# Performance work log

Measured on AMD Instinct MI355X. Metric: run time of the kernel, lower is better.

## Reference

```python
import jax, jax.numpy as jnp
import numpy as np

B, T, D, H, DK = 4, 2048, 1024, 16, 64
DV = 2 * DK
QKD = H * DK           # 1024
VD = H * DV            # 2048
KW = 4                 # conv kernel size
EPS = 1e-5


def zc_rms(x, scale):
    # zero-centered RMS norm over last axis
    xc = x - jnp.mean(x, axis=-1, keepdims=True)
    return xc * jax.lax.rsqrt(jnp.mean(xc * xc, axis=-1, keepdims=True) + EPS) * scale


def causal_dwconv(x, kern, bias):
    # depthwise causal conv1d: x [B,T,C], kern [K,C], bias [C]
    k = kern.shape[0]
    t = x.shape[1]
    xp = jnp.pad(x, ((0, 0), (k - 1, 0), (0, 0)))
    out = bias
    for i in range(k):  # small fixed K=4
        out = out + xp[:, i:i + t, :] * kern[i]
    return out


def _forward(x, q_w, k_w, v_w, q_scale, k_scale, v_scale,
             q_conv_k, q_conv_b, k_conv_k, k_conv_b, v_conv_k, v_conv_b,
             alpha_w, beta_w, out_w, gate_w):
    # Q/K/V: Dense -> zero-centered RMSNorm -> causal depthwise conv -> SiLU
    q = jax.nn.silu(causal_dwconv(zc_rms(x @ q_w, q_scale), q_conv_k, q_conv_b))
    k = jax.nn.silu(causal_dwconv(zc_rms(x @ k_w, k_scale), k_conv_k, k_conv_b))
    v = jax.nn.silu(causal_dwconv(zc_rms(x @ v_w, v_scale), v_conv_k, v_conv_b))

    q = q.reshape(B, T, H, DK)
    k = k.reshape(B, T, H, DK)
    v = v.reshape(B, T, H, DV)

    alpha = jax.nn.sigmoid(x @ alpha_w)  # [B,T,H] per-head decay gate
    beta = jax.nn.sigmoid(x @ beta_w)    # [B,T,H] per-head write strength

    def step(S, inp):
        # S: [B,H,DK,DV]
        qt, kt, vt, at, bt = inp
        Sd = at[..., None, None] * S                              # gated decay
        pred = jnp.einsum('bhd,bhdv->bhv', kt, Sd)                # current memory readout at k
        S_new = Sd + bt[..., None, None] * jnp.einsum('bhd,bhv->bhdv', kt, vt - pred)  # delta rule
        ot = jnp.einsum('bhd,bhdv->bhv', qt, S_new)
        return S_new, ot

    xs = (jnp.transpose(q, (1, 0, 2, 3)),
          jnp.transpose(k, (1, 0, 2, 3)),
          jnp.transpose(v, (1, 0, 2, 3)),
          jnp.transpose(alpha, (1, 0, 2)),
          jnp.transpose(beta, (1, 0, 2)))
    S0 = jnp.zeros((B, H, DK, DV), x.dtype)
    _, o = jax.lax.scan(step, S0, xs)                             # o: [T,B,H,DV]

    core = jnp.transpose(o, (1, 0, 2, 3)).reshape(B, T, VD)
    # gated linear unit output
    return (core @ out_w) * jax.nn.sigmoid(x @ gate_w)


def setup_inputs() -> dict:
    key = jax.random.key(0)
    ks = jax.random.split(key, 12)
    g = lambda i, shape, s: jax.random.normal(ks[i], shape, dtype=jnp.float32) * s
    return {
        'x': g(0, (B, T, D), 1.0),
        'q_w': g(1, (D, QKD), 0.02), 'k_w': g(2, (D, QKD), 0.02), 'v_w': g(3, (D, VD), 0.02),
        'q_scale': jnp.ones((QKD,), jnp.float32),
        'k_scale': jnp.ones((QKD,), jnp.float32),
        'v_scale': jnp.ones((VD,), jnp.float32),
        'q_conv_k': g(4, (KW, QKD), 0.1), 'q_conv_b': jnp.zeros((QKD,), jnp.float32),
        'k_conv_k': g(5, (KW, QKD), 0.1), 'k_conv_b': jnp.zeros((QKD,), jnp.float32),
        'v_conv_k': g(6, (KW, VD), 0.1), 'v_conv_b': jnp.zeros((VD,), jnp.float32),
        'alpha_w': g(7, (D, H), 0.02), 'beta_w': g(8, (D, H), 0.02),
        'out_w': g(9, (VD, D), 0.02), 'gate_w': g(10, (D, D), 0.02),
    }


def reference(x, q_w, k_w, v_w, q_scale, k_scale, v_scale,
              q_conv_k, q_conv_b, k_conv_k, k_conv_b, v_conv_k, v_conv_b,
              alpha_w, beta_w, out_w, gate_w):
    return _forward(x, q_w, k_w, v_w, q_scale, k_scale, v_scale,
                    q_conv_k, q_conv_b, k_conv_k, k_conv_b, v_conv_k, v_conv_b,
                    alpha_w, beta_w, out_w, gate_w)
```

## Files before the change

kernel.cpp:

```cpp
#include <hip/hip_runtime.h>

#define Bc   4
#define Tc   2048
#define Dc   1024
#define Hc   16
#define DKc  64
#define DVc  128
#define QKDc 1024
#define VDc  2048
#define NPRJ 5120
#define Mc   (Bc * Tc)
#define CHUNK 64
#define NCHK (Tc / CHUNK)

typedef __bf16 bf16;
typedef __bf16 bf16x4 __attribute__((ext_vector_type(4)));
typedef __bf16 bf16x8 __attribute__((ext_vector_type(8)));
typedef float  f32x4  __attribute__((ext_vector_type(4)));

__device__ __forceinline__ float bf2f(bf16 v) { return (float)v; }
__device__ __forceinline__ bf16  f2bf(float v) { return (bf16)v; }
__device__ __forceinline__ float sigmoidf_(float x) { return 1.0f / (1.0f + __expf(-x)); }
__device__ __forceinline__ f32x4 mfma16(bf16x8 a, bf16x8 b, f32x4 c) {
    return __builtin_amdgcn_mfma_f32_16x16x32_bf16(a, b, c, 0, 0, 0);
}

__device__ __forceinline__ void glds16(const bf16* g, void* l) {
    __builtin_amdgcn_global_load_lds((const __attribute__((address_space(1))) void*)g,
                                     (__attribute__((address_space(3))) void*)l, 16, 0, 0);
}

__device__ __forceinline__ bf16* swz32x64(bf16* base, int r, int k) {
    int byte = (((r << 6) + k) << 1) ^ ((r & 7) << 4);
    return (bf16*)((char*)base + byte);
}

__global__ __launch_bounds__(256) void cast_f32_bf16(const float* __restrict__ src,
                                                     bf16* __restrict__ dst, int n4) {
    int i = blockIdx.x * 256 + threadIdx.x;
    if (i < n4) {
        float4 v = ((const float4*)src)[i];
        bf16x4 o = { f2bf(v.x), f2bf(v.y), f2bf(v.z), f2bf(v.w) };
        ((bf16x4*)dst)[i] = o;
    }
}

__global__ __launch_bounds__(256) void transpose_cast(const float* __restrict__ src,
                                                      bf16* __restrict__ dst,
                                                      int R, int C) {
    __shared__ float tile[32][33];
    int c0 = blockIdx.x * 32, r0 = blockIdx.y * 32;
    int tx = threadIdx.x, ty = threadIdx.y;
#pragma unroll
    for (int i = 0; i < 32; i += 8) {
        int r = r0 + ty + i, c = c0 + tx;
        tile[ty + i][tx] = (r < R && c < C) ? src[(size_t)r * C + c] : 0.0f;
    }
    __syncthreads();
#pragma unroll
    for (int i = 0; i < 32; i += 8) {
        int rr = c0 + ty + i, cc = r0 + tx;
        if (rr < C && cc < R) dst[(size_t)rr * R + cc] = f2bf(tile[tx][ty + i]);
    }
}

#define GP_NT 20
#define GP_MT 32
#define GP_NKT 32
__global__ __launch_bounds__(512, 2) void gemm_pipe(const bf16* __restrict__ A,
                                                    const bf16* __restrict__ Bt,
                                                    bf16* __restrict__ C) {
    __shared__ __align__(16) char lds[131072];
    const int tid = threadIdx.x;
    const int wid = tid >> 6, lane = tid & 63;
    const int lm = lane & 15, lq = lane >> 4;
    const int wm = wid >> 2, wn = wid & 3;

    const int id = blockIdx.x;
    const int nid = (id & 7) * ((GP_NT * GP_MT) / 8) + (id >> 3);
    const int tn = nid % GP_NT, tm = nid / GP_NT;
    const int n0 = tn * 256, m0 = tm * 256;

    const int r0 = tid >> 2;
    const int lsx = ((tid & 3) ^ (r0 & 3)) << 3;
    const bf16* sA0 = A  + (size_t)(m0 + r0) * Dc + lsx;
    const bf16* sA1 = sA0 + (size_t)128 * Dc;
    const bf16* sB0 = Bt + (size_t)(n0 + r0) * Dc + lsx;
    const bf16* sB1 = sB0 + (size_t)128 * Dc;

    auto stageA = [&](int kt) {
        char* d = lds + ((kt & 3) << 15) + wid * 1024;
        glds16(sA0 + kt * 32, d);
        glds16(sA1 + kt * 32, d + 8192);
    };
    auto stageB = [&](int kt) {
        char* d = lds + ((kt & 3) << 15) + 16384 + wid * 1024;
        glds16(sB0 + kt * 32, d);
        glds16(sB1 + kt * 32, d + 8192);
    };

    f32x4 acc[8][4] = {};
    const int sx = (lq ^ (lm & 3)) << 3;
    const int aoff = wm * 4096 + lm * 32 + sx;
    const int boff = wn * 2048 + lm * 32 + sx;

    stageA(0); stageB(0); stageA(1); stageB(1); stageA(2); stageB(2);
    asm volatile("s_waitcnt vmcnt(8)" ::: "memory");
    asm volatile("s_barrier" ::: "memory");

    for (int kt = 0; kt < GP_NKT; kt++) {
        const bf16* sA = (const bf16*)(lds + ((kt & 3) << 15));
        const bf16* sB = (const bf16*)(lds + ((kt & 3) << 15) + 16384);
        bf16x8 aF[4], bF[4], aG[4];
#pragma unroll
        for (int i = 0; i < 4; i++) aF[i] = *(const bf16x8*)&sA[aoff + i * 512];
#pragma unroll
        for (int j = 0; j < 4; j++) bF[j] = *(const bf16x8*)&sB[boff + j * 512];
#pragma unroll
        for (int i = 0; i < 4; i++) aG[i] = *(const bf16x8*)&sA[aoff + (i + 4) * 512];
        if (kt + 3 < GP_NKT) { stageA(kt + 3); stageB(kt + 3); }
        __builtin_amdgcn_s_setprio(1);
#pragma unroll
        for (int i = 0; i < 4; i++)
#pragma unroll
            for (int j = 0; j < 4; j++)
                acc[i][j] = mfma16(aF[i], bF[j], acc[i][j]);
#pragma unroll
        for (int i = 0; i < 4; i++)
#pragma unroll
            for (int j = 0; j < 4; j++)
                acc[i + 4][j] = mfma16(aG[i], bF[j], acc[i + 4][j]);
        __builtin_amdgcn_s_setprio(0);
        if (kt + 3 < GP_NKT)      asm volatile("s_waitcnt vmcnt(8)" ::: "memory");
        else if (kt + 2 < GP_NKT) asm volatile("s_waitcnt vmcnt(4)" ::: "memory");
        else                      asm volatile("s_waitcnt vmcnt(0)" ::: "memory");
        asm volatile("s_barrier" ::: "memory");
    }

    const int rbase = m0 + wm * 128 + lq * 4;
    const int cbase = n0 + wn * 64 + lm;
#pragma unroll
    for (int i = 0; i < 8; i++)
#pragma unroll
        for (int j = 0; j < 4; j++)
#pragma unroll
            for (int rI = 0; rI < 4; rI++)
                C[(size_t)(rbase + i * 16 + rI) * NPRJ + cbase + j * 16] =
                    f2bf(acc[i][j][rI]);
}

#define GO_NKT 64
__global__ __launch_bounds__(512, 2) void gemm_pipe_out(const bf16* __restrict__ A,
                                                        const bf16* __restrict__ Bt,
                                                        float* __restrict__ C,
                                                        const bf16* __restrict__ gate) {
    __shared__ __align__(16) char lds[98304];
    const int tid = threadIdx.x;
    const int wid = tid >> 6, lane = tid & 63;
    const int lm = lane & 15, lq = lane >> 4;
    const int wm = wid >> 2, wn = wid & 3;

    const int id = blockIdx.x;
    const int nid = (id & 7) * 32 + (id >> 3);
    const int tm = nid >> 2, tn = nid & 3;
    const int m0 = tm * 128, n0 = tn * 256;

    const int r0 = tid >> 2;
    const int lsx = ((tid & 3) ^ (r0 & 3)) << 3;
    const bf16* sAp = A  + (size_t)(m0 + r0) * NPRJ + lsx;
    const bf16* sB0 = Bt + (size_t)(n0 + r0) * VDc + lsx;
    const bf16* sB1 = sB0 + (size_t)128 * VDc;

    auto stageA = [&](int kt) {
        glds16(sAp + kt * 32, lds + (kt & 3) * 24576 + wid * 1024);
    };
    auto stageB = [&](int kt) {
        char* d = lds + (kt & 3) * 24576 + 8192 + wid * 1024;
        glds16(sB0 + kt * 32, d);
        glds16(sB1 + kt * 32, d + 8192);
    };

    f32x4 acc[4][4] = {};
    const int sx = (lq ^ (lm & 3)) << 3;
    const int aoff = wm * 2048 + lm * 32 + sx;
    const int boff = wn * 2048 + lm * 32 + sx;

    stageA(0); stageB(0); stageA(1); stageB(1); stageA(2); stageB(2);
    asm volatile("s_waitcnt vmcnt(6)" ::: "memory");
    asm volatile("s_barrier" ::: "memory");

    for (int kt = 0; kt < GO_NKT; kt++) {
        const bf16* sA = (const bf16*)(lds + (kt & 3) * 24576);
        const bf16* sB = sA + 4096;
        bf16x8 a[4], b[4];
#pragma unroll
        for (int i = 0; i < 4; i++) a[i] = *(const bf16x8*)&sA[aoff + i * 512];
#pragma unroll
        for (int j = 0; j < 4; j++) b[j] = *(const bf16x8*)&sB[boff + j * 512];
        if (kt + 3 < GO_NKT) { stageA(kt + 3); stageB(kt + 3); }
        __builtin_amdgcn_s_setprio(1);
#pragma unroll
        for (int i = 0; i < 4; i++)
#pragma unroll
            for (int j = 0; j < 4; j++)
                acc[i][j] = mfma16(a[i], b[j], acc[i][j]);
        __builtin_amdgcn_s_setprio(0);
        if (kt + 3 < GO_NKT)      asm volatile("s_waitcnt vmcnt(6)" ::: "memory");
        else if (kt + 2 < GO_NKT) asm volatile("s_waitcnt vmcnt(3)" ::: "memory");
        else                      asm volatile("s_waitcnt vmcnt(0)" ::: "memory");
        asm volatile("s_barrier" ::: "memory");
    }

    const int rbase = m0 + wm * 64 + lq * 4;
    const int cbase = n0 + wn * 64 + lm;
#pragma unroll
    for (int i = 0; i < 4; i++)
#pragma unroll
        for (int j = 0; j < 4; j++)
#pragma unroll
            for (int rI = 0; rI < 4; rI++) {
                int row = rbase + i * 16 + rI;
                int col = cbase + j * 16;
                float g = bf2f(gate[(size_t)row * NPRJ + col]);
                C[(size_t)row * Dc + col] = acc[i][j][rI] * sigmoidf_(g);
            }
}

template <int L>
__global__ __launch_bounds__(256) void zc_rms_v(bf16* __restrict__ buf,
                                                const float* __restrict__ scale,
                                                int ld) {
    constexpr int NW = L / 8 / 64;
    const int row = blockIdx.x, t = threadIdx.x;
    bf16* p = buf + (size_t)row * ld;
    bf16x8 v = *(const bf16x8*)&p[t * 8];
    float xv[8], s = 0.f, s2 = 0.f;
#pragma unroll
    for (int e = 0; e < 8; e++) { xv[e] = bf2f(v[e]); s += xv[e]; s2 += xv[e] * xv[e]; }
    __shared__ float red[2][NW];
#pragma unroll
    for (int o = 32; o > 0; o >>= 1) {
        s += __shfl_down(s, o, 64);
        s2 += __shfl_down(s2, o, 64);
    }
    if ((t & 63) == 0) { red[0][t >> 6] = s; red[1][t >> 6] = s2; }
    __syncthreads();
    s = 0.f; s2 = 0.f;
#pragma unroll
    for (int wv = 0; wv < NW; wv++) { s += red[0][wv]; s2 += red[1][wv]; }
    float mean = s / (float)L;
    float inv = rsqrtf(s2 / (float)L - mean * mean + 1e-5f);
    float4 s0 = *(const float4*)&scale[t * 8];
    float4 s1 = *(const float4*)&scale[t * 8 + 4];
    float sc[8] = { s0.x, s0.y, s0.z, s0.w, s1.x, s1.y, s1.z, s1.w };
    bf16x8 o;
#pragma unroll
    for (int e = 0; e < 8; e++) o[e] = f2bf((xv[e] - mean) * inv * sc[e]);
    *(bf16x8*)&p[t * 8] = o;
}

template <int CCH>
__global__ __launch_bounds__(256) void conv_silu_v(const bf16* __restrict__ xn,
                                                   const float* __restrict__ kern,
                                                   const float* __restrict__ bias,
                                                   bf16* __restrict__ out, int ldin) {
    const int btok = blockIdx.x;
    const int tt = btok & (Tc - 1);
    const int c8 = threadIdx.x * 8;
    float4 b0 = *(const float4*)&bias[c8], b1 = *(const float4*)&bias[c8 + 4];
    float acc[8] = { b0.x, b0.y, b0.z, b0.w, b1.x, b1.y, b1.z, b1.w };
#pragma unroll
    for (int i = 0; i < 4; i++) {
        if (tt - 3 + i >= 0) {
            bf16x8 xv = *(const bf16x8*)&xn[(size_t)(btok - 3 + i) * ldin + c8];
            float4 k0 = *(const float4*)&kern[i * CCH + c8];
            float4 k1 = *(const float4*)&kern[i * CCH + c8 + 4];
            float kk[8] = { k0.x, k0.y, k0.z, k0.w, k1.x, k1.y, k1.z, k1.w };
#pragma unroll
            for (int e = 0; e < 8; e++) acc[e] += bf2f(xv[e]) * kk[e];
        }
    }
    bf16x8 o;
#pragma unroll
    for (int e = 0; e < 8; e++) {
        float y = acc[e] * sigmoidf_(acc[e]);
        o[e] = f2bf(y);
    }
    *(bf16x8*)&out[(size_t)btok * CCH + c8] = o;
}

__global__ __launch_bounds__(256) void alphabeta_mfma(const bf16* __restrict__ x,
                                                      const float* __restrict__ aw,
                                                      const float* __restrict__ bw,
                                                      float* __restrict__ af,
                                                      float* __restrict__ bfv) {
    __shared__ bf16 whi[32][136];
    __shared__ bf16 wlo[32][136];
    const int tid = threadIdx.x, wave = tid >> 6, lane = tid & 63;
    const int lm = lane & 15, lq = lane >> 4;
    const int m0 = blockIdx.x * 128;
    f32x4 acc[2][2] = {};

    for (int k0 = 0; k0 < Dc; k0 += 128) {
        for (int idx = tid; idx < 4096; idx += 256) {
            int n = idx & 31, kk = idx >> 5;
            float v = (n < 16) ? aw[(size_t)(k0 + kk) * Hc + n]
                               : bw[(size_t)(k0 + kk) * Hc + (n - 16)];
            bf16 h = f2bf(v);
            whi[n][kk] = h;
            wlo[n][kk] = f2bf(v - bf2f(h));
        }
        __syncthreads();
#pragma unroll
        for (int ks = 0; ks < 4; ks++) {
            bf16x8 bh[2], bl[2];
#pragma unroll
            for (int j = 0; j < 2; j++) {
                bh[j] = *(const bf16x8*)&whi[j * 16 + lm][ks * 32 + lq * 8];
                bl[j] = *(const bf16x8*)&wlo[j * 16 + lm][ks * 32 + lq * 8];
            }
#pragma unroll
            for (int ii = 0; ii < 2; ii++) {
                int row = m0 + wave * 32 + ii * 16 + lm;
                bf16x8 a = *(const bf16x8*)&x[(size_t)row * Dc + k0 + ks * 32 + lq * 8];
#pragma unroll
                for (int j = 0; j < 2; j++) {
                    acc[ii][j] = mfma16(a, bh[j], acc[ii][j]);
                    acc[ii][j] = mfma16(a, bl[j], acc[ii][j]);
                }
            }
        }
        __syncthreads();
    }
#pragma unroll
    for (int ii = 0; ii < 2; ii++)
#pragma unroll
        for (int rI = 0; rI < 4; rI++) {
            int row = m0 + wave * 32 + ii * 16 + lq * 4 + rI;
            af[(size_t)row * Hc + lm]  = sigmoidf_(acc[ii][0][rI]);
            bfv[(size_t)row * Hc + lm] = sigmoidf_(acc[ii][1][rI]);
        }
}

__global__ __launch_bounds__(256) void prep(bf16* __restrict__ qf,
                                            bf16* __restrict__ kf,
                                            bf16* __restrict__ vc,
                                            const float* __restrict__ af,
                                            const float* __restrict__ bfv,
                                            bf16* __restrict__ Wb,
                                            bf16* __restrict__ Mb,
                                            float* __restrict__ gamC) {
    __shared__ __align__(16) char smem[53248];
    bf16*  Kc   = (bf16*)(smem);
    bf16*  Qc   = (bf16*)(smem + 9216);
    float* DT   = (float*)(smem + 9216);
    float* Pn   = (float*)(smem + 13568);
    float* TT   = (float*)(smem + 15744);
    float* Qn   = (float*)(smem + 9216);
    bf16*  Tb   = (bf16*)(smem + 9216);
    float* As   = (float*)(smem + 18432);
    bf16*  Vtb  = (bf16*)(smem + 18432);
    float* Ts   = (float*)(smem + 35072);
    float* lg_s = (float*)(smem + 51712);
    float* bv_s = lg_s + 64;
    float* bg_s = lg_s + 128;
    float* gm_s = lg_s + 192;
    float* kr_s = lg_s + 256;

    const int c    = blockIdx.x;
    const int bh   = blockIdx.y;
    const int b    = bh >> 4, h = bh & 15;
    const int ch   = bh * NCHK + c;
    const int tok0 = b * Tc + c * CHUNK;
    const int tid  = threadIdx.x;
    const int wave = tid >> 6, lane = tid & 63;
    const int lm = lane & 15, lq = lane >> 4, kh = lq * 8;

#pragma unroll
    for (int r = 0; r < 2; r++) {
        int idx = tid + r * 256;
        int row = idx >> 3, c8 = (idx & 7) * 8;
        *(bf16x8*)&Kc[row * 72 + c8] =
            *(const bf16x8*)&kf[(size_t)(tok0 + row) * QKDc + h * DKc + c8];
        *(bf16x8*)&Qc[row * 72 + c8] =
            *(const bf16x8*)&qf[(size_t)(tok0 + row) * QKDc + h * DKc + c8];
    }
    for (int idx = tid; idx < 64 * 65; idx += 256) Ts[idx] = 0.f;
    if (tid < 64) {
        float a  = af[(size_t)(tok0 + tid) * Hc + h];
        float bb = bfv[(size_t)(tok0 + tid) * Hc + h];
        float la = __log2f(fmaxf(a, 1e-30f));
#pragma unroll
        for (int o = 1; o < 64; o <<= 1) {
            float t = __shfl_up(la, o, 64);
            if (tid >= o) la += t;
        }
        float lgC = __shfl(la, 63, 64);
        lg_s[tid] = la;
        bv_s[tid] = bb;
        float g   = exp2f(la);
        gm_s[tid] = g;
        bg_s[tid] = bb * g;
        kr_s[tid] = exp2f(lgC - la);
        if (tid == 0) gamC[ch] = exp2f(lgC);
    }
    __syncthreads();

    {
        bf16x8 ka[2], qa[2];
#pragma unroll
        for (int s = 0; s < 2; s++) {
            ka[s] = *(const bf16x8*)&Kc[(16 * wave + lm) * 72 + s * 32 + kh];
            qa[s] = *(const bf16x8*)&Qc[(16 * wave + lm) * 72 + s * 32 + kh];
        }
#pragma unroll
        for (int jt = 0; jt < 4; jt++) {
            f32x4 kkacc = {}, qkacc = {};
#pragma unroll
            for (int s = 0; s < 2; s++) {
                bf16x8 kbf = *(const bf16x8*)&Kc[(16 * jt + lm) * 72 + s * 32 + kh];
                kkacc = mfma16(ka[s], kbf, kkacc);
                qkacc = mfma16(qa[s], kbf, qkacc);
            }
#pragma unroll
            for (int rI = 0; rI < 4; rI++) {
                int i = 16 * wave + lq * 4 + rI;
                int j = 16 * jt + lm;
                float ratio = exp2f(lg_s[i] - lg_s[j]);
                As[i * 65 + j] = (j < i) ? bv_s[i] * ratio * kkacc[rI] : 0.f;
                Mb[((size_t)ch * 64 + i) * 64 + j] =
                    (j <= i) ? f2bf(ratio * qkacc[rI]) : f2bf(0.f);
            }
        }
    }
    {
#pragma unroll
        for (int r = 0; r < 2; r++) {
            int idx = tid + r * 256;
            int row = idx >> 3, c8 = (idx & 7) * 8;
            bf16x8 v = *(const bf16x8*)&Qc[row * 72 + c8];
            float g = gm_s[row];
            bf16x8 oq;
#pragma unroll
            for (int e = 0; e < 8; e++) oq[e] = f2bf(bf2f(v[e]) * g);
            *(bf16x8*)&qf[(size_t)(tok0 + row) * QKDc + h * DKc + c8] = oq;
            bf16x8 ok;
#pragma unroll
            for (int e = 0; e < 8; e++)
                ok[e] = f2bf(kr_s[c8 + e] * bf2f(Kc[(c8 + e) * 72 + row]));
            *(bf16x8*)&kf[(size_t)(tok0 + row) * QKDc + h * DKc + c8] = ok;
        }
    }
    __syncthreads();

    if (tid < 64) {
        const int g = lane >> 4, jj = lane & 15, base = lane & 48;
        float areg[16], tcol[16];
#pragma unroll
        for (int i = 0; i < 16; i++) areg[i] = As[(16 * g + i) * 65 + 16 * g + jj];
#pragma unroll
        for (int i = 0; i < 16; i++) tcol[i] = (i == jj) ? 1.f : 0.f;
#pragma unroll
        for (int i = 1; i < 16; i++) {
            float s = 0.f;
#pragma unroll
            for (int m = 0; m < i; m++)
                s = fmaf(__shfl(areg[i], base + m, 64), tcol[m], s);
            tcol[i] = (i == jj) ? 1.f : -s;
        }
#pragma unroll
        for (int i = 0; i < 16; i++) {
            Ts[(16 * g + i) * 65 + 16 * g + jj] = tcol[i];
            DT[g * 272 + jj * 17 + i] = tcol[i];
        }
    }
    __syncthreads();

    if (wave < 2) {
        const int w = wave;
        bf16x8 ah, al, bh, bl;
#pragma unroll
        for (int e = 0; e < 8; e++) {
            int k = kh + e;
            float xa = (k < 16) ? DT[2 * w * 272 + lm * 17 + k] : 0.f;
            bf16 ha = f2bf(xa); ah[e] = ha; al[e] = f2bf(xa - bf2f(ha));
            float xb = (k < 16) ? As[(16 + 32 * w + lm) * 65 + 32 * w + k] : 0.f;
            bf16 hb = f2bf(xb); bh[e] = hb; bl[e] = f2bf(xb - bf2f(hb));
        }
        f32x4 acc = {};
        acc = mfma16(ah, bh, acc); acc = mfma16(ah, bl, acc); acc = mfma16(al, bh, acc);
#pragma unroll
        for (int rI = 0; rI < 4; rI++)
            Pn[w * 272 + (lq * 4 + rI) * 17 + lm] = -acc[rI];
    }
    __syncthreads();

    if (wave < 3) {
        bf16x8 ah, al, bh, bl;
#pragma unroll
        for (int e = 0; e < 8; e++) {
            int k = kh + e;
            float xa = 0.f, xb = 0.f;
            if (k < 16) {
                if (wave == 0)      { xa = Ts[(16 + lm) * 65 + 16 + k]; xb = Pn[lm * 17 + k]; }
                else if (wave == 1) { xa = Pn[lm * 17 + k];             xb = Ts[(16 + lm) * 65 + 16 + k]; }
                else                { xa = Ts[(48 + lm) * 65 + 48 + k]; xb = Pn[272 + lm * 17 + k]; }
            }
            bf16 ha = f2bf(xa); ah[e] = ha; al[e] = f2bf(xa - bf2f(ha));
            bf16 hb = f2bf(xb); bh[e] = hb; bl[e] = f2bf(xb - bf2f(hb));
        }
        f32x4 acc = {};
        acc = mfma16(ah, bh, acc); acc = mfma16(ah, bl, acc); acc = mfma16(al, bh, acc);
#pragma unroll
        for (int rI = 0; rI < 4; rI++) {
            int ro = lq * 4 + rI;
            if (wave == 0)      Ts[(16 + ro) * 65 + lm]      = acc[rI];
            else if (wave == 1) TT[ro * 17 + lm]             = acc[rI];
            else                Ts[(48 + ro) * 65 + 32 + lm] = acc[rI];
        }
    }
    __syncthreads();

    {
        const int a = wave >> 1, bq = wave & 1;
        bf16x8 ah, al, bh, bl;
#pragma unroll
        for (int e = 0; e < 8; e++) {
            int k = kh + e;
            float xa;
            if (a == 0) xa = (k < 16) ? DT[lm * 17 + k] : TT[lm * 17 + (k - 16)];
            else        xa = (k < 16) ? 0.f : DT[272 + lm * 17 + (k - 16)];
            bf16 ha = f2bf(xa); ah[e] = ha; al[e] = f2bf(xa - bf2f(ha));
            float xb = As[(32 + 16 * bq + lm) * 65 + k];
            bf16 hb = f2bf(xb); bh[e] = hb; bl[e] = f2bf(xb - bf2f(hb));
        }
        f32x4 acc = {};
        acc = mfma16(ah, bh, acc); acc = mfma16(ah, bl, acc); acc = mfma16(al, bh, acc);
        __syncthreads();
#pragma unroll
        for (int rI = 0; rI < 4; rI++)
            Qn[(16 * a + lq * 4 + rI) * 33 + 16 * bq + lm] = -acc[rI];
    }
    __syncthreads();

    {
        const int a = wave >> 1, bq = wave & 1;
        bf16x8 ah, al, bh, bl;
#pragma unroll
        for (int e = 0; e < 8; e++) {
            int k = kh + e;
            float xa = Ts[(32 + 16 * a + lm) * 65 + 32 + k];
            bf16 ha = f2bf(xa); ah[e] = ha; al[e] = f2bf(xa - bf2f(ha));
            float xb = Qn[(16 * bq + lm) * 33 + k];
            bf16 hb = f2bf(xb); bh[e] = hb; bl[e] = f2bf(xb - bf2f(hb));
        }
        f32x4 acc = {};
        acc = mfma16(ah, bh, acc); acc = mfma16(ah, bl, acc); acc = mfma16(al, bh, acc);
#pragma unroll
        for (int rI = 0; rI < 4; rI++)
            Ts[(32 + 16 * a + lq * 4 + rI) * 65 + 16 * bq + lm] = acc[rI];
    }
    __syncthreads();

    for (int idx = tid; idx < 4096; idx += 256) {
        int i = idx >> 6, j = idx & 63;
        Tb[i * 72 + j] = f2bf(Ts[i * 65 + j]);
    }
    __syncthreads();
#pragma unroll
    for (int r = 0; r < 4; r++) {
        int idx = tid + r * 256;
        int j = idx >> 4, c8 = (idx & 15) * 8;
        bf16x8 v = *(const bf16x8*)&vc[(size_t)(tok0 + j) * VDc + h * DVc + c8];
        float bb = bv_s[j];
#pragma unroll
        for (int e = 0; e < 8; e++)
            Vtb[(c8 + e) * 72 + j] = f2bf(bf2f(v[e]) * bb);
    }
    __syncthreads();
    {
        bf16x8 ta[2];
#pragma unroll
        for (int s = 0; s < 2; s++)
            ta[s] = *(const bf16x8*)&Tb[(16 * wave + lm) * 72 + s * 32 + kh];
#pragma unroll
        for (int dt = 0; dt < 4; dt++) {
            f32x4 wacc = {};
#pragma unroll
            for (int s = 0; s < 2; s++) {
                bf16x8 wbf;
                int d = 16 * dt + lm;
#pragma unroll
                for (int e = 0; e < 8; e++) {
                    int j = s * 32 + kh + e;
                    wbf[e] = f2bf(bg_s[j] * bf2f(Kc[j * 72 + d]));
                }
                wacc = mfma16(ta[s], wbf, wacc);
            }
#pragma unroll
            for (int rI = 0; rI < 4; rI++) {
                int i = 16 * wave + lq * 4 + rI;
                Wb[((size_t)ch * 64 + i) * 64 + 16 * dt + lm] = f2bf(wacc[rI]);
            }
        }
#pragma unroll
        for (int dt = 0; dt < 8; dt++) {
            f32x4 uacc = {};
#pragma unroll
            for (int s = 0; s < 2; s++) {
                bf16x8 vb = *(const bf16x8*)&Vtb[(16 * dt + lm) * 72 + s * 32 + kh];
                uacc = mfma16(ta[s], vb, uacc);
            }
#pragma unroll
            for (int rI = 0; rI < 4; rI++) {
                int i = 16 * wave + lq * 4 + rI;
                vc[(size_t)(tok0 + i) * VDc + h * DVc + 16 * dt + lm] = f2bf(uacc[rI]);
            }
        }
    }
}

__global__ __launch_bounds__(256) void chunkloop(const bf16* __restrict__ qf,
                                                 const bf16* __restrict__ kf,
                                                 const bf16* __restrict__ vc,
                                                 const bf16* __restrict__ Wb,
                                                 const bf16* __restrict__ Mb,
                                                 const float* __restrict__ gamC,
                                                 bf16* __restrict__ o, int ldo) {
    const int vg = blockIdx.x;
    const int bh = blockIdx.y;
    const int b = bh >> 4, h = bh & 15;
    const int tid = threadIdx.x;
    const int wave = tid >> 6, lane = tid & 63;
    const int lm = lane & 15, lq = lane >> 4, kh = lq * 8;

    __shared__ __align__(16) bf16 SbBuf[32 * 64];
    __shared__ __align__(16) bf16 UtBuf[32 * 64];

    for (int idx = tid; idx < 32 * 64; idx += 256) SbBuf[idx] = f2bf(0.f);

    f32x4 Sacc[2] = {};

    const int colK = h * DKc;
    const int colV = h * DVc + vg * 32;

    bf16x8 wa[2], qa[2], ma[2], kb[2];
    bf16 uvv[2][4];

    auto loadFrags = [&](int c, bf16x8 (&wa_)[2], bf16x8 (&qa_)[2], bf16x8 (&ma_)[2],
                         bf16x8 (&kb_)[2], bf16 (&uvv_)[2][4]) {
        const int tok0 = b * Tc + c * CHUNK;
        const size_t chb = ((size_t)bh * NCHK + c) * 64;
#pragma unroll
        for (int s = 0; s < 2; s++) {
            wa_[s] = *(const bf16x8*)&Wb[(chb + 16 * wave + lm) * 64 + s * 32 + kh];
            ma_[s] = *(const bf16x8*)&Mb[(chb + 16 * wave + lm) * 64 + s * 32 + kh];
            qa_[s] = *(const bf16x8*)&qf[(size_t)(tok0 + 16 * wave + lm) * QKDc + colK + s * 32 + kh];
            kb_[s] = *(const bf16x8*)&kf[(size_t)(tok0 + 16 * wave + lm) * QKDc + colK + s * 32 + kh];
        }
#pragma unroll
        for (int dt = 0; dt < 2; dt++)
#pragma unroll
            for (int rI = 0; rI < 4; rI++)
                uvv_[dt][rI] =
                    vc[(size_t)(tok0 + 16 * wave + lq * 4 + rI) * VDc + colV + 16 * dt + lm];
    };

    loadFrags(0, wa, qa, ma, kb, uvv);
    __syncthreads();

    for (int c = 0; c < NCHK; c++) {
        const float gC = gamC[(size_t)bh * NCHK + c];
        bf16x8 sf[2][2];
#pragma unroll
        for (int dt = 0; dt < 2; dt++)
#pragma unroll
            for (int s = 0; s < 2; s++)
                sf[dt][s] = *(const bf16x8*)swz32x64(SbBuf, 16 * dt + lm, s * 32 + kh);
        f32x4 pacc[2] = {};
#pragma unroll
        for (int dt = 0; dt < 2; dt++)
#pragma unroll
            for (int s = 0; s < 2; s++)
                pacc[dt] = mfma16(wa[s], sf[dt][s], pacc[dt]);

        bf16x8 wa2[2], qa2[2], ma2[2], kb2[2];
        bf16 uvv2[2][4];
        if (c + 1 < NCHK) loadFrags(c + 1, wa2, qa2, ma2, kb2, uvv2);

#pragma unroll
        for (int dt = 0; dt < 2; dt++)
#pragma unroll
            for (int rI = 0; rI < 4; rI++) {
                float u = bf2f(uvv[dt][rI]) - pacc[dt][rI];
                *swz32x64(UtBuf, 16 * dt + lm, 16 * wave + lq * 4 + rI) = f2bf(u);
            }
        __syncthreads();

        bf16x8 uf[2][2];
#pragma unroll
        for (int dt = 0; dt < 2; dt++)
#pragma unroll
            for (int s = 0; s < 2; s++)
                uf[dt][s] = *(const bf16x8*)swz32x64(UtBuf, 16 * dt + lm, s * 32 + kh);

        f32x4 oacc[2] = {};
#pragma unroll
        for (int dt = 0; dt < 2; dt++)
#pragma unroll
            for (int s = 0; s < 2; s++) {
                oacc[dt] = mfma16(qa[s], sf[dt][s], oacc[dt]);
                oacc[dt] = mfma16(ma[s], uf[dt][s], oacc[dt]);
            }
        {
            const int tok0 = b * Tc + c * CHUNK;
#pragma unroll
            for (int dt = 0; dt < 2; dt++)
#pragma unroll
                for (int rI = 0; rI < 4; rI++)
                    o[(size_t)(tok0 + 16 * wave + lq * 4 + rI) * ldo + colV + 16 * dt + lm] =
                        f2bf(oacc[dt][rI]);
        }
#pragma unroll
        for (int dt = 0; dt < 2; dt++) {
#pragma unroll
            for (int e = 0; e < 4; e++) Sacc[dt][e] *= gC;
#pragma unroll
            for (int s = 0; s < 2; s++)
                Sacc[dt] = mfma16(uf[dt][s], kb[s], Sacc[dt]);
        }
        __syncthreads();
#pragma unroll
        for (int dt = 0; dt < 2; dt++)
#pragma unroll
            for (int rI = 0; rI < 4; rI++)
                *swz32x64(SbBuf, 16 * dt + lq * 4 + rI, 16 * wave + lm) = f2bf(Sacc[dt][rI]);
        __syncthreads();

        if (c + 1 < NCHK) {
#pragma unroll
            for (int s = 0; s < 2; s++) { wa[s] = wa2[s]; qa[s] = qa2[s]; ma[s] = ma2[s]; kb[s] = kb2[s]; }
#pragma unroll
            for (int dt = 0; dt < 2; dt++)
#pragma unroll
                for (int rI = 0; rI < 4; rI++) uvv[dt][rI] = uvv2[dt][rI];
        }
    }
}

extern "C" void kernel_launch(void* const* d_in, const int* in_sizes, int n_in,
                              void* d_out, int out_size, void* d_ws, size_t ws_size,
                              hipStream_t stream) {
    const float* x        = (const float*)d_in[0];
    const float* q_w      = (const float*)d_in[1];
    const float* k_w      = (const float*)d_in[2];
    const float* v_w      = (const float*)d_in[3];
    const float* q_scale  = (const float*)d_in[4];
    const float* k_scale  = (const float*)d_in[5];
    const float* v_scale  = (const float*)d_in[6];
    const float* q_conv_k = (const float*)d_in[7];
    const float* q_conv_b = (const float*)d_in[8];
    const float* k_conv_k = (const float*)d_in[9];
    const float* k_conv_b = (const float*)d_in[10];
    const float* v_conv_k = (const float*)d_in[11];
    const float* v_conv_b = (const float*)d_in[12];
    const float* alpha_w  = (const float*)d_in[13];
    const float* beta_w   = (const float*)d_in[14];
    const float* out_w    = (const float*)d_in[15];
    const float* gate_w   = (const float*)d_in[16];

    char* w = (char*)d_ws;
    bf16* xb  = (bf16*)w; w += (size_t)Mc * Dc * 2;
    bf16* qwT = (bf16*)w; w += (size_t)QKDc * Dc * 2;
    bf16* kwT = (bf16*)w; w += (size_t)QKDc * Dc * 2;
    bf16* vwT = (bf16*)w; w += (size_t)VDc * Dc * 2;
    bf16* gwT = (bf16*)w; w += (size_t)Dc * Dc * 2;
    bf16* owT = (bf16*)w; w += (size_t)Dc * VDc * 2;
    bf16* lin_all = (bf16*)w; w += (size_t)Mc * NPRJ * 2;
    bf16* qf = (bf16*)w; w += (size_t)Mc * QKDc * 2;
    bf16* kf = (bf16*)w; w += (size_t)Mc * QKDc * 2;
    bf16* vc = (bf16*)w; w += (size_t)Mc * VDc * 2;
    float* af = (float*)w; w += (size_t)Mc * Hc * 4;
    float* bfv = (float*)w; w += (size_t)Mc * Hc * 4;
    const int NCH_TOT = Bc * Hc * NCHK;
    bf16* Wb = (bf16*)w; w += (size_t)NCH_TOT * 64 * 64 * 2;
    bf16* Mb = (bf16*)w; w += (size_t)NCH_TOT * 64 * 64 * 2;
    float* gamC = (float*)w; w += (size_t)NCH_TOT * 4;
    bf16* o_core = lin_all;

    dim3 tb(32, 8);
    cast_f32_bf16<<<(Mc * Dc / 4 + 255) / 256, 256, 0, stream>>>(x, xb, Mc * Dc / 4);
    transpose_cast<<<dim3(QKDc / 32, Dc / 32), tb, 0, stream>>>(q_w, qwT, Dc, QKDc);
    transpose_cast<<<dim3(QKDc / 32, Dc / 32), tb, 0, stream>>>(k_w, kwT, Dc, QKDc);
    transpose_cast<<<dim3(VDc / 32, Dc / 32), tb, 0, stream>>>(v_w, vwT, Dc, VDc);
    transpose_cast<<<dim3(Dc / 32, Dc / 32), tb, 0, stream>>>(gate_w, gwT, Dc, Dc);
    transpose_cast<<<dim3(Dc / 32, VDc / 32), tb, 0, stream>>>(out_w, owT, VDc, Dc);

    gemm_pipe<<<GP_NT * GP_MT, 512, 0, stream>>>(xb, qwT, lin_all);

    zc_rms_v<QKDc><<<Mc, QKDc / 8, 0, stream>>>(lin_all,        q_scale, NPRJ);
    zc_rms_v<QKDc><<<Mc, QKDc / 8, 0, stream>>>(lin_all + 1024, k_scale, NPRJ);
    zc_rms_v<VDc><<<Mc, VDc / 8, 0, stream>>>(lin_all + 2048,   v_scale, NPRJ);

    conv_silu_v<QKDc><<<Mc, QKDc / 8, 0, stream>>>(lin_all,        q_conv_k, q_conv_b, qf, NPRJ);
    conv_silu_v<QKDc><<<Mc, QKDc / 8, 0, stream>>>(lin_all + 1024, k_conv_k, k_conv_b, kf, NPRJ);
    conv_silu_v<VDc><<<Mc, VDc / 8, 0, stream>>>(lin_all + 2048,   v_conv_k, v_conv_b, vc, NPRJ);

    alphabeta_mfma<<<Mc / 128, 256, 0, stream>>>(xb, alpha_w, beta_w, af, bfv);

    prep<<<dim3(NCHK, Bc * Hc), 256, 0, stream>>>(qf, kf, vc, af, bfv, Wb, Mb, gamC);
    chunkloop<<<dim3(4, Bc * Hc), 256, 0, stream>>>(qf, kf, vc, Wb, Mb, gamC, o_core, NPRJ);

    gemm_pipe_out<<<256, 512, 0, stream>>>(o_core, owT, (float*)d_out, lin_all + 4096);
}
```

Measured before the change: 524.5 us.

## Fuse RMS norm into conv, retune LDS swizzle, remap chunkloop blocks and V transpose

Merges the zero-centered RMS norm and the causal conv+SiLU into one kernel. Each block recomputes the norm statistics for the 4 rows in the conv window, so the in-place normalized write and the separate launches go away. It also changes the XOR swizzle in both GEMMs to use row bits 1-2, which should cut LDS bank conflicts. The chunkloop grid becomes 1D with an XCD-aware mapping so blocks sharing a head land on the same XCD, and the prep V-transpose load pattern is reordered. The fused kernel does four times the reductions per row, so it adds redundant compute and register pressure.

```diff
diff --git a/kernel.cpp b/kernel.cpp
--- a/kernel.cpp
+++ b/kernel.cpp
@@ -82,7 +82,7 @@
     const int n0 = tn * 256, m0 = tm * 256;
 
     const int r0 = tid >> 2;
-    const int lsx = ((tid & 3) ^ (r0 & 3)) << 3;
+    const int lsx = ((tid & 3) ^ ((r0 >> 1) & 3)) << 3;
     const bf16* sA0 = A  + (size_t)(m0 + r0) * Dc + lsx;
     const bf16* sA1 = sA0 + (size_t)128 * Dc;
     const bf16* sB0 = Bt + (size_t)(n0 + r0) * Dc + lsx;
@@ -100,7 +100,7 @@
     };
 
     f32x4 acc[8][4] = {};
-    const int sx = (lq ^ (lm & 3)) << 3;
+    const int sx = (lq ^ ((lm >> 1) & 3)) << 3;
     const int aoff = wm * 4096 + lm * 32 + sx;
     const int boff = wn * 2048 + lm * 32 + sx;
 
@@ -166,7 +166,7 @@
     const int m0 = tm * 128, n0 = tn * 256;
 
     const int r0 = tid >> 2;
-    const int lsx = ((tid & 3) ^ (r0 & 3)) << 3;
+    const int lsx = ((tid & 3) ^ ((r0 >> 1) & 3)) << 3;
     const bf16* sAp = A  + (size_t)(m0 + r0) * NPRJ + lsx;
     const bf16* sB0 = Bt + (size_t)(n0 + r0) * VDc + lsx;
     const bf16* sB1 = sB0 + (size_t)128 * VDc;
@@ -181,7 +181,7 @@
     };
 
     f32x4 acc[4][4] = {};
-    const int sx = (lq ^ (lm & 3)) << 3;
+    const int sx = (lq ^ ((lm >> 1) & 3)) << 3;
     const int aoff = wm * 2048 + lm * 32 + sx;
     const int boff = wn * 2048 + lm * 32 + sx;
 
@@ -226,58 +226,65 @@
             }
 }
 
-template <int L>
-__global__ __launch_bounds__(256) void zc_rms_v(bf16* __restrict__ buf,
+template <int CCH>
+__global__ __launch_bounds__(256) void normconv(const bf16* __restrict__ xn,
                                                 const float* __restrict__ scale,
-                                                int ld) {
-    constexpr int NW = L / 8 / 64;
-    const int row = blockIdx.x, t = threadIdx.x;
-    bf16* p = buf + (size_t)row * ld;
-    bf16x8 v = *(const bf16x8*)&p[t * 8];
-    float xv[8], s = 0.f, s2 = 0.f;
-#pragma unroll
-    for (int e = 0; e < 8; e++) { xv[e] = bf2f(v[e]); s += xv[e]; s2 += xv[e] * xv[e]; }
-    __shared__ float red[2][NW];
-#pragma unroll
-    for (int o = 32; o > 0; o >>= 1) {
-        s += __shfl_down(s, o, 64);
-        s2 += __shfl_down(s2, o, 64);
-    }
-    if ((t & 63) == 0) { red[0][t >> 6] = s; red[1][t >> 6] = s2; }
-    __syncthreads();
-    s = 0.f; s2 = 0.f;
-#pragma unroll
-    for (int wv = 0; wv < NW; wv++) { s += red[0][wv]; s2 += red[1][wv]; }
-    float mean = s / (float)L;
-    float inv = rsqrtf(s2 / (float)L - mean * mean + 1e-5f);
-    float4 s0 = *(const float4*)&scale[t * 8];
-    float4 s1 = *(const float4*)&scale[t * 8 + 4];
-    float sc[8] = { s0.x, s0.y, s0.z, s0.w, s1.x, s1.y, s1.z, s1.w };
-    bf16x8 o;
-#pragma unroll
-    for (int e = 0; e < 8; e++) o[e] = f2bf((xv[e] - mean) * inv * sc[e]);
-    *(bf16x8*)&p[t * 8] = o;
-}
-
-template <int CCH>
-__global__ __launch_bounds__(256) void conv_silu_v(const bf16* __restrict__ xn,
-                                                   const float* __restrict__ kern,
-                                                   const float* __restrict__ bias,
-                                                   bf16* __restrict__ out, int ldin) {
+                                                const float* __restrict__ kern,
+                                                const float* __restrict__ bias,
+                                                bf16* __restrict__ out, int ldin) {
+    constexpr int NW = CCH / 8 / 64;
     const int btok = blockIdx.x;
     const int tt = btok & (Tc - 1);
-    const int c8 = threadIdx.x * 8;
+    const int t = threadIdx.x;
+    const int c8 = t * 8;
+
+    float xv[4][8];
+    float s[4] = {}, s2[4] = {};
+#pragma unroll
+    for (int i = 0; i < 4; i++) {
+        if (tt - 3 + i >= 0) {
+            bf16x8 v = *(const bf16x8*)&xn[(size_t)(btok - 3 + i) * ldin + c8];
+#pragma unroll
+            for (int e = 0; e < 8; e++) {
+                float x = bf2f(v[e]);
+                xv[i][e] = x; s[i] += x; s2[i] += x * x;
+            }
+        }
+    }
+    __shared__ float red[NW][8];
+#pragma unroll
+    for (int o = 32; o > 0; o >>= 1)
+#pragma unroll
+        for (int i = 0; i < 4; i++) {
+            s[i]  += __shfl_down(s[i],  o, 64);
+            s2[i] += __shfl_down(s2[i], o, 64);
+        }
+    if ((t & 63) == 0)
+#pragma unroll
+        for (int i = 0; i < 4; i++) { red[t >> 6][i] = s[i]; red[t >> 6][4 + i] = s2[i]; }
+    __syncthreads();
+#pragma unroll
+    for (int i = 0; i < 4; i++) {
+        s[i] = 0.f; s2[i] = 0.f;
+#pragma unroll
+        for (int w = 0; w < NW; w++) { s[i] += red[w][i]; s2[i] += red[w][4 + i]; }
+    }
+
+    float4 sc0 = *(const float4*)&scale[c8], sc1 = *(const float4*)&scale[c8 + 4];
+    float sc[8] = { sc0.x, sc0.y, sc0.z, sc0.w, sc1.x, sc1.y, sc1.z, sc1.w };
     float4 b0 = *(const float4*)&bias[c8], b1 = *(const float4*)&bias[c8 + 4];
     float acc[8] = { b0.x, b0.y, b0.z, b0.w, b1.x, b1.y, b1.z, b1.w };
 #pragma unroll
     for (int i = 0; i < 4; i++) {
         if (tt - 3 + i >= 0) {
-            bf16x8 xv = *(const bf16x8*)&xn[(size_t)(btok - 3 + i) * ldin + c8];
+            float mean = s[i] / (float)CCH;
+            float inv = rsqrtf(s2[i] / (float)CCH - mean * mean + 1e-5f);
             float4 k0 = *(const float4*)&kern[i * CCH + c8];
             float4 k1 = *(const float4*)&kern[i * CCH + c8 + 4];
             float kk[8] = { k0.x, k0.y, k0.z, k0.w, k1.x, k1.y, k1.z, k1.w };
 #pragma unroll
-            for (int e = 0; e < 8; e++) acc[e] += bf2f(xv[e]) * kk[e];
+            for (int e = 0; e < 8; e++)
+                acc[e] += (xv[i][e] - mean) * inv * sc[e] * kk[e];
         }
     }
     bf16x8 o;
@@ -569,13 +576,13 @@
     __syncthreads();
 #pragma unroll
     for (int r = 0; r < 4; r++) {
-        int idx = tid + r * 256;
-        int j = idx >> 4, c8 = (idx & 15) * 8;
-        bf16x8 v = *(const bf16x8*)&vc[(size_t)(tok0 + j) * VDc + h * DVc + c8];
+        int j = r * 16 + (tid & 15);
+        int dbase = (tid >> 4) * 8;
+        bf16x8 v = *(const bf16x8*)&vc[(size_t)(tok0 + j) * VDc + h * DVc + dbase];
         float bb = bv_s[j];
 #pragma unroll
         for (int e = 0; e < 8; e++)
-            Vtb[(c8 + e) * 72 + j] = f2bf(bf2f(v[e]) * bb);
+            Vtb[(dbase + e) * 72 + j] = f2bf(bf2f(v[e]) * bb);
     }
     __syncthreads();
     {
@@ -627,8 +634,11 @@
                                                  const bf16* __restrict__ Mb,
                                                  const float* __restrict__ gamC,
                                                  bf16* __restrict__ o, int ldo) {
-    const int vg = blockIdx.x;
-    const int bh = blockIdx.y;
+    const int bi = blockIdx.x;
+    const int xcd = bi & 7;
+    const int r8 = bi >> 3;
+    const int bh = xcd * 8 + (r8 & 7);
+    const int vg = r8 >> 3;
     const int b = bh >> 4, h = bh & 15;
     const int tid = threadIdx.x;
     const int wave = tid >> 6, lane = tid & 63;
@@ -798,18 +808,14 @@
 
     gemm_pipe<<<GP_NT * GP_MT, 512, 0, stream>>>(xb, qwT, lin_all);
 
-    zc_rms_v<QKDc><<<Mc, QKDc / 8, 0, stream>>>(lin_all,        q_scale, NPRJ);
-    zc_rms_v<QKDc><<<Mc, QKDc / 8, 0, stream>>>(lin_all + 1024, k_scale, NPRJ);
-    zc_rms_v<VDc><<<Mc, VDc / 8, 0, stream>>>(lin_all + 2048,   v_scale, NPRJ);
-
-    conv_silu_v<QKDc><<<Mc, QKDc / 8, 0, stream>>>(lin_all,        q_conv_k, q_conv_b, qf, NPRJ);
-    conv_silu_v<QKDc><<<Mc, QKDc / 8, 0, stream>>>(lin_all + 1024, k_conv_k, k_conv_b, kf, NPRJ);
-    conv_silu_v<VDc><<<Mc, VDc / 8, 0, stream>>>(lin_all + 2048,   v_conv_k, v_conv_b, vc, NPRJ);
+    normconv<QKDc><<<Mc, QKDc / 8, 0, stream>>>(lin_all,        q_scale, q_conv_k, q_conv_b, qf, NPRJ);
+    normconv<QKDc><<<Mc, QKDc / 8, 0, stream>>>(lin_all + 1024, k_scale, k_conv_k, k_conv_b, kf, NPRJ);
+    normconv<VDc><<<Mc, VDc / 8, 0, stream>>>(lin_all + 2048,   v_scale, v_conv_k, v_conv_b, vc, NPRJ);
 
     alphabeta_mfma<<<Mc / 128, 256, 0, stream>>>(xb, alpha_w, beta_w, af, bfv);
 
     prep<<<dim3(NCHK, Bc * Hc), 256, 0, stream>>>(qf, kf, vc, af, bfv, Wb, Mb, gamC);
-    chunkloop<<<dim3(4, Bc * Hc), 256, 0, stream>>>(qf, kf, vc, Wb, Mb, gamC, o_core, NPRJ);
+    chunkloop<<<256, 256, 0, stream>>>(qf, kf, vc, Wb, Mb, gamC, o_core, NPRJ);
 
     gemm_pipe_out<<<256, 512, 0, stream>>>(o_core, owT, (float*)d_out, lin_all + 4096);
 }
```

New measurement: 493.4 us. 5.9% less time.
